# Kernel optimization log

Hardware: AMD Instinct MI355X
Metric: run time of the kernel (lower is better)

The kernel has to match this reference:

```python
import jax, jax.numpy as jnp
import numpy as np

N_EMBED = 384
NUM_HEADS = 6
HEAD_SIZE = N_EMBED // NUM_HEADS  # 64
B, T = 8, 2048


def setup_inputs() -> dict:
    key = jax.random.key(0)
    ks = jax.random.split(key, 8)
    s = 1.0 / np.sqrt(N_EMBED)
    query = jax.random.normal(ks[0], (B, T, N_EMBED), dtype=jnp.float32)
    key_t = jax.random.normal(ks[1], (B, T, N_EMBED), dtype=jnp.float32)
    value = jax.random.normal(ks[2], (B, T, N_EMBED), dtype=jnp.float32)
    # causal-style mask, broadcastable over (B, H)
    mask = jnp.tril(jnp.ones((T, T), dtype=jnp.int32))[None, None]
    Wk = jax.random.normal(ks[3], (N_EMBED, N_EMBED), dtype=jnp.float32) * s
    Wq = jax.random.normal(ks[4], (N_EMBED, N_EMBED), dtype=jnp.float32) * s
    Wv = jax.random.normal(ks[5], (N_EMBED, N_EMBED), dtype=jnp.float32) * s
    Wproj = jax.random.normal(ks[6], (N_EMBED, N_EMBED), dtype=jnp.float32) * s
    bproj = jnp.zeros((N_EMBED,), dtype=jnp.float32)
    return {"query": query, "key": key_t, "value": value, "mask": mask,
            "Wk": Wk, "Wq": Wq, "Wv": Wv, "Wproj": Wproj, "bproj": bproj}


def _split_heads(x):
    b, t, c = x.shape
    return x.reshape(b, t, NUM_HEADS, c // NUM_HEADS).transpose(0, 2, 1, 3)  # [B,H,T,D]


def reference(query, key, value, mask, Wk, Wq, Wv, Wproj, bproj):
    b, t, c = query.shape
    # NOTE: source swaps names: k = key_proj(query), q = query_proj(key)
    k = _split_heads(query @ Wk.T)
    q = _split_heads(key @ Wq.T)
    v = _split_heads(value @ Wv.T)
    # scale by full C (not head_size), as in the source
    wei = jnp.einsum("bhqd,bhkd->bhqk", q, k) * (c ** -0.5)
    # masked_fill with 0 BEFORE softmax (faithful to source)
    wei = jnp.where(mask == 0, jnp.float32(0.0), wei)
    wei = jax.nn.softmax(wei, axis=-1)
    out = jnp.einsum("bhqk,bhkd->bhqd", wei, v)
    out = out.transpose(0, 2, 1, 3).reshape(b, t, c)
    out = out @ Wproj.T + bproj  # dropout is identity at inference
    return out
```

## Files before the change

### kernel.cpp

```cpp
#include <hip/hip_runtime.h>
#include <hip/hip_bf16.h>


#define TT 2048
#define CC 384
#define HH 6
#define DD 64
#define SCALE 0.05103103630798288f

typedef __bf16 bf16x8 __attribute__((ext_vector_type(8)));
typedef __bf16 bf16x4 __attribute__((ext_vector_type(4)));
typedef float f32x4 __attribute__((ext_vector_type(4)));

__device__ __forceinline__ int swz(int row, int byteInRow) {
    return row * 128 + (byteInRow ^ ((row & 7) << 4));
}

__global__ __launch_bounds__(256) void qkv_proj_kernel(
    const float* __restrict__ query, const float* __restrict__ key,
    const float* __restrict__ value, const float* __restrict__ Wk,
    const float* __restrict__ Wq, const float* __restrict__ Wv,
    __bf16* __restrict__ Kb, __bf16* __restrict__ Qb, __bf16* __restrict__ VTb)
{
    __shared__ __align__(16) char smem[49152];

    const int tid = threadIdx.x;
    const int wid = tid >> 6, lane = tid & 63;
    const int lrow = lane & 15, g = lane >> 4;
    const int pid = blockIdx.z;
    const int m0 = blockIdx.x * 128, n0 = blockIdx.y * 64;
    const float* X = (pid == 0) ? query : ((pid == 1) ? key : value);
    const float* W = (pid == 0) ? Wk : ((pid == 1) ? Wq : Wv);

    const int xrow = tid >> 4, xcol = (tid & 15) * 4;
    const float* xp = X + (size_t)(m0 + xrow) * CC + xcol;
    const float* wp = W + (size_t)(n0 + (tid >> 4)) * CC + xcol;

    f32x4 xr[8], wr[4];

    f32x4 acc[2][4];
#pragma unroll
    for (int i = 0; i < 2; ++i)
#pragma unroll
        for (int j = 0; j < 4; ++j) acc[i][j] = (f32x4){0.f, 0.f, 0.f, 0.f};

#pragma unroll
    for (int i = 0; i < 8; ++i) xr[i] = *(const f32x4*)(xp + (size_t)i * 16 * CC);
#pragma unroll
    for (int i = 0; i < 4; ++i) wr[i] = *(const f32x4*)(wp + (size_t)i * 16 * CC);
    {
        char* Xd = smem;
        char* Wd = smem + 32768;
#pragma unroll
        for (int i = 0; i < 8; ++i) {
            bf16x4 hh;
            hh[0] = (__bf16)xr[i][0]; hh[1] = (__bf16)xr[i][1];
            hh[2] = (__bf16)xr[i][2]; hh[3] = (__bf16)xr[i][3];
            *(bf16x4*)(Xd + swz(xrow + i * 16, xcol * 2)) = hh;
        }
#pragma unroll
        for (int i = 0; i < 4; ++i) {
            bf16x4 hh;
            hh[0] = (__bf16)wr[i][0]; hh[1] = (__bf16)wr[i][1];
            hh[2] = (__bf16)wr[i][2]; hh[3] = (__bf16)wr[i][3];
            *(bf16x4*)(Wd + swz((tid >> 4) + i * 16, xcol * 2)) = hh;
        }
    }
    __syncthreads();

    int cur = 0;
    for (int kk = 0; kk < 6; ++kk) {
        if (kk < 5) {
            const int k0 = (kk + 1) * 64;
#pragma unroll
            for (int i = 0; i < 8; ++i) xr[i] = *(const f32x4*)(xp + (size_t)i * 16 * CC + k0);
#pragma unroll
            for (int i = 0; i < 4; ++i) wr[i] = *(const f32x4*)(wp + (size_t)i * 16 * CC + k0);
        }
        const char* Xs = smem + cur * 16384;
        const char* Ws = smem + 32768 + cur * 8192;

        __builtin_amdgcn_s_setprio(1);
        if (pid < 2) {
#pragma unroll
            for (int kc = 0; kc < 2; ++kc) {
                int kb = kc * 64 + g * 16;
                bf16x8 a0 = *(bf16x8*)(Xs + swz(wid * 32 + lrow, kb));
                bf16x8 a1 = *(bf16x8*)(Xs + swz(wid * 32 + 16 + lrow, kb));
#pragma unroll
                for (int nf = 0; nf < 4; ++nf) {
                    bf16x8 b = *(bf16x8*)(Ws + swz(nf * 16 + lrow, kb));
                    acc[0][nf] = __builtin_amdgcn_mfma_f32_16x16x32_bf16(a0, b, acc[0][nf], 0, 0, 0);
                    acc[1][nf] = __builtin_amdgcn_mfma_f32_16x16x32_bf16(a1, b, acc[1][nf], 0, 0, 0);
                }
            }
        } else {
#pragma unroll
            for (int kc = 0; kc < 2; ++kc) {
                int kb = kc * 64 + g * 16;
                bf16x8 b0 = *(bf16x8*)(Xs + swz(wid * 32 + lrow, kb));
                bf16x8 b1 = *(bf16x8*)(Xs + swz(wid * 32 + 16 + lrow, kb));
#pragma unroll
                for (int nf = 0; nf < 4; ++nf) {
                    bf16x8 a = *(bf16x8*)(Ws + swz(nf * 16 + lrow, kb));
                    acc[0][nf] = __builtin_amdgcn_mfma_f32_16x16x32_bf16(a, b0, acc[0][nf], 0, 0, 0);
                    acc[1][nf] = __builtin_amdgcn_mfma_f32_16x16x32_bf16(a, b1, acc[1][nf], 0, 0, 0);
                }
            }
        }
        __builtin_amdgcn_s_setprio(0);

        if (kk < 5) {
            char* Xd = smem + (cur ^ 1) * 16384;
            char* Wd = smem + 32768 + (cur ^ 1) * 8192;
#pragma unroll
            for (int i = 0; i < 8; ++i) {
                bf16x4 hh;
                hh[0] = (__bf16)xr[i][0]; hh[1] = (__bf16)xr[i][1];
                hh[2] = (__bf16)xr[i][2]; hh[3] = (__bf16)xr[i][3];
                *(bf16x4*)(Xd + swz(xrow + i * 16, xcol * 2)) = hh;
            }
#pragma unroll
            for (int i = 0; i < 4; ++i) {
                bf16x4 hh;
                hh[0] = (__bf16)wr[i][0]; hh[1] = (__bf16)wr[i][1];
                hh[2] = (__bf16)wr[i][2]; hh[3] = (__bf16)wr[i][3];
                *(bf16x4*)(Wd + swz((tid >> 4) + i * 16, xcol * 2)) = hh;
            }
        }
        __syncthreads();
        cur ^= 1;
    }

    if (pid < 2) {
        __bf16* out = (pid == 0) ? Kb : Qb;
#pragma unroll
        for (int mf = 0; mf < 2; ++mf)
#pragma unroll
            for (int nf = 0; nf < 4; ++nf)
#pragma unroll
                for (int r = 0; r < 4; ++r) {
                    int m = m0 + wid * 32 + mf * 16 + g * 4 + r;
                    int n = n0 + nf * 16 + lrow;
                    int b = m >> 11, t = m & 2047, h = n >> 6, d = n & 63;
                    out[((size_t)(b * HH + h) * TT + t) * DD + d] = (__bf16)acc[mf][nf][r];
                }
    } else {
#pragma unroll
        for (int mf = 0; mf < 2; ++mf)
#pragma unroll
            for (int nf = 0; nf < 4; ++nf)
#pragma unroll
                for (int r = 0; r < 4; ++r) {
                    int n = n0 + nf * 16 + g * 4 + r;
                    int m = m0 + wid * 32 + mf * 16 + lrow;
                    int b = m >> 11, t = m & 2047, h = n >> 6, d = n & 63;
                    VTb[((size_t)(b * HH + h) * DD + d) * TT + t] = (__bf16)acc[mf][nf][r];
                }
    }
}

__global__ __launch_bounds__(256) void suffix_kernel(
    const __bf16* __restrict__ VTb, float* __restrict__ Ssuf)
{
    __shared__ float tsum[4][32];
    const int bh = blockIdx.x;
    const int tid = threadIdx.x, wid = tid >> 6, lane = tid & 63;

#pragma unroll
    for (int it = 0; it < 4; ++it) {
        const int dr = blockIdx.y * 16 + wid * 4 + it;
        const __bf16* src = VTb + (size_t)(bh * DD + dr) * TT;
#pragma unroll
        for (int step = 0; step < 4; ++step) {
            bf16x8 v = *(const bf16x8*)(src + step * 512 + lane * 8);
            float sacc = 0.f;
#pragma unroll
            for (int i = 0; i < 8; ++i) sacc += (float)v[i];
            sacc += __shfl_xor(sacc, 1);
            sacc += __shfl_xor(sacc, 2);
            sacc += __shfl_xor(sacc, 4);
            if ((lane & 7) == 0) tsum[wid][step * 8 + (lane >> 3)] = sacc;
        }
        float s2 = 0.f;
        for (int j = 0; j < 32; ++j) {
            float tv = tsum[wid][j];
            if (j >= lane) s2 += tv;
        }
        if (lane <= 32) Ssuf[(size_t)(bh * 33 + lane) * 64 + dr] = s2;
    }
}

__global__ __launch_bounds__(256) void attn_kernel(
    const __bf16* __restrict__ Qb, const __bf16* __restrict__ Kb,
    const __bf16* __restrict__ VTb, const float* __restrict__ Ssuf,
    __bf16* __restrict__ attn)
{
    __shared__ __align__(16) char smem[32768];
    const int tid = threadIdx.x;
    const int wid = tid >> 6, lane = tid & 63;
    const int lrow = lane & 15, g = lane >> 4;

    const int i = blockIdx.x;
    const int j = i >> 3;
    const int bh = (i & 7) * 6 + (j >> 4);
    const int Qt = 15 - (j & 15);
    const int q0 = Qt * 128;
    const int nkt = 2 * Qt + 2;

    const int qloc = wid * 32 + lrow;
    const __bf16* qp = Qb + ((size_t)bh * TT + q0 + qloc) * DD + g * 8;
    bf16x8 qb[2][2];
    qb[0][0] = *(const bf16x8*)(qp);
    qb[0][1] = *(const bf16x8*)(qp + 32);
    qb[1][0] = *(const bf16x8*)(qp + 16 * DD);
    qb[1][1] = *(const bf16x8*)(qp + 16 * DD + 32);

    const int r0 = tid >> 3;
    const int c8 = (tid & 7) * 8;
    const __bf16* kbase = Kb + (size_t)bh * TT * DD;
    const __bf16* vbase = VTb + (size_t)bh * DD * TT;

    bf16x8 kr0, kr1, vr0, vr1;

    f32x4 o[2][4];
#pragma unroll
    for (int mf = 0; mf < 2; ++mf)
#pragma unroll
        for (int ds = 0; ds < 4; ++ds) o[mf][ds] = (f32x4){0.f, 0.f, 0.f, 0.f};
    float z0 = 0.f, z1 = 0.f;

    kr0 = *(const bf16x8*)(kbase + (size_t)r0 * DD + c8);
    kr1 = *(const bf16x8*)(kbase + (size_t)(r0 + 32) * DD + c8);
    vr0 = *(const bf16x8*)(vbase + (size_t)r0 * TT + c8);
    vr1 = *(const bf16x8*)(vbase + (size_t)(r0 + 32) * TT + c8);
    {
        char* Kd = smem;
        char* Vd = smem + 16384;
        *(bf16x8*)(Kd + swz(r0, c8 * 2)) = kr0;
        *(bf16x8*)(Kd + swz(r0 + 32, c8 * 2)) = kr1;
        *(bf16x8*)(Vd + swz(r0, c8 * 2)) = vr0;
        *(bf16x8*)(Vd + swz(r0 + 32, c8 * 2)) = vr1;
    }
    __syncthreads();

    int cur = 0;
    for (int kt = 0; kt < nkt; ++kt) {
        if (kt + 1 < nkt) {
            const int n0 = (kt + 1) * 64;
            kr0 = *(const bf16x8*)(kbase + (size_t)(n0 + r0) * DD + c8);
            kr1 = *(const bf16x8*)(kbase + (size_t)(n0 + r0 + 32) * DD + c8);
            vr0 = *(const bf16x8*)(vbase + (size_t)r0 * TT + n0 + c8);
            vr1 = *(const bf16x8*)(vbase + (size_t)(r0 + 32) * TT + n0 + c8);
        }
        const char* Kc = smem + cur * 8192;
        const char* Vc = smem + 16384 + cur * 8192;
        const bool dm = (kt >= 2 * Qt);

#pragma unroll
        for (int mf = 0; mf < 2; ++mf) {
            f32x4 st[4];
#pragma unroll
            for (int j16 = 0; j16 < 4; ++j16) st[j16] = (f32x4){0.f, 0.f, 0.f, 0.f};
            __builtin_amdgcn_s_setprio(1);
#pragma unroll
            for (int kc = 0; kc < 2; ++kc) {
                bf16x8 qf = qb[mf][kc];
#pragma unroll
                for (int j16 = 0; j16 < 4; ++j16) {
                    bf16x8 kf = *(bf16x8*)(Kc + swz(j16 * 16 + lrow, kc * 64 + g * 16));
                    st[j16] = __builtin_amdgcn_mfma_f32_16x16x32_bf16(kf, qf, st[j16], 0, 0, 0);
                }
            }
            __builtin_amdgcn_s_setprio(0);

            const int qg = q0 + qloc + mf * 16;
            bf16x8 pb0, pb1;
            float zz = 0.f;
#pragma unroll
            for (int j16 = 0; j16 < 4; ++j16) {
#pragma unroll
                for (int r = 0; r < 4; ++r) {
                    float p;
                    if (dm && (kt * 64 + j16 * 16 + g * 4 + r > qg)) p = 1.0f;
                    else p = __expf(st[j16][r] * SCALE);
                    zz += p;
                    if (j16 < 2) pb0[(j16 & 1) * 4 + r] = (__bf16)p;
                    else         pb1[(j16 & 1) * 4 + r] = (__bf16)p;
                }
            }
            if (mf == 0) z0 += zz; else z1 += zz;

            __builtin_amdgcn_s_setprio(1);
#pragma unroll
            for (int kc = 0; kc < 2; ++kc) {
                bf16x8 pf = kc ? pb1 : pb0;
#pragma unroll
                for (int ds = 0; ds < 4; ++ds) {
                    union { bf16x8 v8; bf16x4 h[2]; } vf;
                    vf.h[0] = *(bf16x4*)(Vc + swz(ds * 16 + lrow, kc * 64 + 8 * g));
                    vf.h[1] = *(bf16x4*)(Vc + swz(ds * 16 + lrow, kc * 64 + 8 * g + 32));
                    o[mf][ds] = __builtin_amdgcn_mfma_f32_16x16x32_bf16(vf.v8, pf, o[mf][ds], 0, 0, 0);
                }
            }
            __builtin_amdgcn_s_setprio(0);
        }

        if (kt + 1 < nkt) {
            char* Kd = smem + (cur ^ 1) * 8192;
            char* Vd = smem + 16384 + (cur ^ 1) * 8192;
            *(bf16x8*)(Kd + swz(r0, c8 * 2)) = kr0;
            *(bf16x8*)(Kd + swz(r0 + 32, c8 * 2)) = kr1;
            *(bf16x8*)(Vd + swz(r0, c8 * 2)) = vr0;
            *(bf16x8*)(Vd + swz(r0 + 32, c8 * 2)) = vr1;
        }
        __syncthreads();
        cur ^= 1;
    }

    const float fut = (float)(TT - nkt * 64);
    z0 += __shfl_xor(z0, 16); z0 += __shfl_xor(z0, 32);
    z1 += __shfl_xor(z1, 16); z1 += __shfl_xor(z1, 32);
    const float inv0 = 1.0f / (z0 + fut);
    const float inv1 = 1.0f / (z1 + fut);

    const float* suf = Ssuf + ((size_t)bh * 33 + nkt) * 64;
    const int b = bh / HH, h = bh % HH;
#pragma unroll
    for (int mf = 0; mf < 2; ++mf) {
        const int t = q0 + qloc + mf * 16;
        const float inv = mf ? inv1 : inv0;
        __bf16* orow = attn + ((size_t)(b * TT + t)) * CC + h * DD;
#pragma unroll
        for (int ds = 0; ds < 4; ++ds) {
            f32x4 sv = *(const f32x4*)(suf + ds * 16 + g * 4);
            bf16x4 w;
#pragma unroll
            for (int r = 0; r < 4; ++r) w[r] = (__bf16)((o[mf][ds][r] + sv[r]) * inv);
            *(bf16x4*)(orow + ds * 16 + g * 4) = w;
        }
    }
}

__global__ __launch_bounds__(256) void out_proj_kernel(
    const __bf16* __restrict__ A, const float* __restrict__ W,
    const float* __restrict__ bias, float* __restrict__ out)
{
    __shared__ __align__(16) char smem[49152];
    const int tid = threadIdx.x;
    const int wid = tid >> 6, lane = tid & 63;
    const int lrow = lane & 15, g = lane >> 4;
    const int m0 = blockIdx.x * 128, n0 = blockIdx.y * 64;

    const int arow = tid >> 3, ac8 = (tid & 7) * 8;
    const __bf16* ap = A + (size_t)(m0 + arow) * CC + ac8;
    const int wrow = tid >> 4, wcol = (tid & 15) * 4;
    const float* wp = W + (size_t)(n0 + wrow) * CC + wcol;

    bf16x8 ar[4];
    f32x4 wr[4];

    f32x4 acc[2][4];
#pragma unroll
    for (int i = 0; i < 2; ++i)
#pragma unroll
        for (int j = 0; j < 4; ++j) acc[i][j] = (f32x4){0.f, 0.f, 0.f, 0.f};

#pragma unroll
    for (int i = 0; i < 4; ++i) ar[i] = *(const bf16x8*)(ap + (size_t)i * 32 * CC);
#pragma unroll
    for (int i = 0; i < 4; ++i) wr[i] = *(const f32x4*)(wp + (size_t)i * 16 * CC);
    {
        char* Ad = smem;
        char* Wd = smem + 32768;
#pragma unroll
        for (int i = 0; i < 4; ++i)
            *(bf16x8*)(Ad + swz(arow + i * 32, ac8 * 2)) = ar[i];
#pragma unroll
        for (int i = 0; i < 4; ++i) {
            bf16x4 hh;
            hh[0] = (__bf16)wr[i][0]; hh[1] = (__bf16)wr[i][1];
            hh[2] = (__bf16)wr[i][2]; hh[3] = (__bf16)wr[i][3];
            *(bf16x4*)(Wd + swz(wrow + i * 16, wcol * 2)) = hh;
        }
    }
    __syncthreads();

    int cur = 0;
    for (int kk = 0; kk < 6; ++kk) {
        if (kk < 5) {
            const int k0 = (kk + 1) * 64;
#pragma unroll
            for (int i = 0; i < 4; ++i) ar[i] = *(const bf16x8*)(ap + (size_t)i * 32 * CC + k0);
#pragma unroll
            for (int i = 0; i < 4; ++i) wr[i] = *(const f32x4*)(wp + (size_t)i * 16 * CC + k0);
        }
        const char* Xs = smem + cur * 16384;
        const char* Ws = smem + 32768 + cur * 8192;

        __builtin_amdgcn_s_setprio(1);
#pragma unroll
        for (int kc = 0; kc < 2; ++kc) {
            int kb = kc * 64 + g * 16;
            bf16x8 a0 = *(bf16x8*)(Xs + swz(wid * 32 + lrow, kb));
            bf16x8 a1 = *(bf16x8*)(Xs + swz(wid * 32 + 16 + lrow, kb));
#pragma unroll
            for (int nf = 0; nf < 4; ++nf) {
                bf16x8 b = *(bf16x8*)(Ws + swz(nf * 16 + lrow, kb));
                acc[0][nf] = __builtin_amdgcn_mfma_f32_16x16x32_bf16(a0, b, acc[0][nf], 0, 0, 0);
                acc[1][nf] = __builtin_amdgcn_mfma_f32_16x16x32_bf16(a1, b, acc[1][nf], 0, 0, 0);
            }
        }
        __builtin_amdgcn_s_setprio(0);

        if (kk < 5) {
            char* Ad = smem + (cur ^ 1) * 16384;
            char* Wd = smem + 32768 + (cur ^ 1) * 8192;
#pragma unroll
            for (int i = 0; i < 4; ++i)
                *(bf16x8*)(Ad + swz(arow + i * 32, ac8 * 2)) = ar[i];
#pragma unroll
            for (int i = 0; i < 4; ++i) {
                bf16x4 hh;
                hh[0] = (__bf16)wr[i][0]; hh[1] = (__bf16)wr[i][1];
                hh[2] = (__bf16)wr[i][2]; hh[3] = (__bf16)wr[i][3];
                *(bf16x4*)(Wd + swz(wrow + i * 16, wcol * 2)) = hh;
            }
        }
        __syncthreads();
        cur ^= 1;
    }

#pragma unroll
    for (int nf = 0; nf < 4; ++nf) {
        float bv = bias[n0 + nf * 16 + lrow];
#pragma unroll
        for (int mf = 0; mf < 2; ++mf)
#pragma unroll
            for (int r = 0; r < 4; ++r) {
                int m = m0 + wid * 32 + mf * 16 + g * 4 + r;
                out[(size_t)m * CC + n0 + nf * 16 + lrow] = acc[mf][nf][r] + bv;
            }
    }
}

extern "C" void kernel_launch(void* const* d_in, const int* in_sizes, int n_in,
                              void* d_out, int out_size, void* d_ws, size_t ws_size,
                              hipStream_t stream)
{
    (void)in_sizes; (void)n_in; (void)out_size; (void)ws_size;
    const float* query = (const float*)d_in[0];
    const float* key   = (const float*)d_in[1];
    const float* value = (const float*)d_in[2];
    const float* Wk    = (const float*)d_in[4];
    const float* Wq    = (const float*)d_in[5];
    const float* Wv    = (const float*)d_in[6];
    const float* Wproj = (const float*)d_in[7];
    const float* bproj = (const float*)d_in[8];
    float* out = (float*)d_out;

    char* ws = (char*)d_ws;
    const size_t SZ = 12582912;
    __bf16* Qb   = (__bf16*)(ws);
    __bf16* Kb   = (__bf16*)(ws + SZ);
    __bf16* VTb  = (__bf16*)(ws + 2 * SZ);
    __bf16* Ab   = (__bf16*)(ws + 3 * SZ);
    float*  Ssuf = (float*)(ws + 4 * SZ);

    qkv_proj_kernel<<<dim3(128, 6, 3), 256, 0, stream>>>(query, key, value,
                                                         Wk, Wq, Wv, Kb, Qb, VTb);
    suffix_kernel<<<dim3(48, 4), 256, 0, stream>>>(VTb, Ssuf);
    attn_kernel<<<dim3(768), 256, 0, stream>>>(Qb, Kb, VTb, Ssuf, Ab);
    out_proj_kernel<<<dim3(128, 6), 256, 0, stream>>>(Ab, Wproj, bproj, out);
}
```

Measured before the change: 274.2 us.

## Hoist K/V fragment loads to registers, reorder block mapping, use exp2

```diff
diff --git a/kernel.cpp b/kernel.cpp
--- a/kernel.cpp
+++ b/kernel.cpp
@@ -7,6 +7,7 @@
 #define HH 6
 #define DD 64
 #define SCALE 0.05103103630798288f
+#define SCALE2 0.07362223f
 
 typedef __bf16 bf16x8 __attribute__((ext_vector_type(8)));
 typedef __bf16 bf16x4 __attribute__((ext_vector_type(4)));
@@ -191,7 +192,7 @@
     }
 }
 
-__global__ __launch_bounds__(256) void attn_kernel(
+__global__ __launch_bounds__(256, 3) void attn_kernel(
     const __bf16* __restrict__ Qb, const __bf16* __restrict__ Kb,
     const __bf16* __restrict__ VTb, const float* __restrict__ Ssuf,
     __bf16* __restrict__ attn)
@@ -202,9 +203,11 @@
     const int lrow = lane & 15, g = lane >> 4;
 
     const int i = blockIdx.x;
+    const int xcd = i & 7;
     const int j = i >> 3;
-    const int bh = (i & 7) * 6 + (j >> 4);
-    const int Qt = 15 - (j & 15);
+    const int rank = j / 6;
+    const int bh = xcd * 6 + (j % 6);
+    const int Qt = 15 - rank;
     const int q0 = Qt * 128;
     const int nkt = 2 * Qt + 2;
 
@@ -257,23 +260,42 @@
         const char* Vc = smem + 16384 + cur * 8192;
         const bool dm = (kt >= 2 * Qt);
 
+        bf16x8 kfr[2][4];
+#pragma unroll
+        for (int kc = 0; kc < 2; ++kc)
+#pragma unroll
+            for (int j16 = 0; j16 < 4; ++j16)
+                kfr[kc][j16] = *(const bf16x8*)(Kc + swz(j16 * 16 + lrow, kc * 64 + g * 16));
+
+        f32x4 st[2][4];
+#pragma unroll
+        for (int mf = 0; mf < 2; ++mf)
+#pragma unroll
+            for (int j16 = 0; j16 < 4; ++j16) st[mf][j16] = (f32x4){0.f, 0.f, 0.f, 0.f};
+        __builtin_amdgcn_s_setprio(1);
+#pragma unroll
+        for (int kc = 0; kc < 2; ++kc)
+#pragma unroll
+            for (int mf = 0; mf < 2; ++mf)
+#pragma unroll
+                for (int j16 = 0; j16 < 4; ++j16)
+                    st[mf][j16] = __builtin_amdgcn_mfma_f32_16x16x32_bf16(
+                        kfr[kc][j16], qb[mf][kc], st[mf][j16], 0, 0, 0);
+        __builtin_amdgcn_s_setprio(0);
+
+        bf16x8 vfr[2][4];
+#pragma unroll
+        for (int kc = 0; kc < 2; ++kc)
+#pragma unroll
+            for (int ds = 0; ds < 4; ++ds) {
+                union { bf16x8 v8; bf16x4 h[2]; } u;
+                u.h[0] = *(const bf16x4*)(Vc + swz(ds * 16 + lrow, kc * 64 + 8 * g));
+                u.h[1] = *(const bf16x4*)(Vc + swz(ds * 16 + lrow, kc * 64 + 8 * g + 32));
+                vfr[kc][ds] = u.v8;
+            }
+
 #pragma unroll
         for (int mf = 0; mf < 2; ++mf) {
-            f32x4 st[4];
-#pragma unroll
-            for (int j16 = 0; j16 < 4; ++j16) st[j16] = (f32x4){0.f, 0.f, 0.f, 0.f};
-            __builtin_amdgcn_s_setprio(1);
-#pragma unroll
-            for (int kc = 0; kc < 2; ++kc) {
-                bf16x8 qf = qb[mf][kc];
-#pragma unroll
-                for (int j16 = 0; j16 < 4; ++j16) {
-                    bf16x8 kf = *(bf16x8*)(Kc + swz(j16 * 16 + lrow, kc * 64 + g * 16));
-                    st[j16] = __builtin_amdgcn_mfma_f32_16x16x32_bf16(kf, qf, st[j16], 0, 0, 0);
-                }
-            }
-            __builtin_amdgcn_s_setprio(0);
-
             const int qg = q0 + qloc + mf * 16;
             bf16x8 pb0, pb1;
             float zz = 0.f;
@@ -283,7 +305,7 @@
                 for (int r = 0; r < 4; ++r) {
                     float p;
                     if (dm && (kt * 64 + j16 * 16 + g * 4 + r > qg)) p = 1.0f;
-                    else p = __expf(st[j16][r] * SCALE);
+                    else p = exp2f(st[mf][j16][r] * SCALE2);
                     zz += p;
                     if (j16 < 2) pb0[(j16 & 1) * 4 + r] = (__bf16)p;
                     else         pb1[(j16 & 1) * 4 + r] = (__bf16)p;
@@ -296,12 +318,9 @@
             for (int kc = 0; kc < 2; ++kc) {
                 bf16x8 pf = kc ? pb1 : pb0;
 #pragma unroll
-                for (int ds = 0; ds < 4; ++ds) {
-                    union { bf16x8 v8; bf16x4 h[2]; } vf;
-                    vf.h[0] = *(bf16x4*)(Vc + swz(ds * 16 + lrow, kc * 64 + 8 * g));
-                    vf.h[1] = *(bf16x4*)(Vc + swz(ds * 16 + lrow, kc * 64 + 8 * g + 32));
-                    o[mf][ds] = __builtin_amdgcn_mfma_f32_16x16x32_bf16(vf.v8, pf, o[mf][ds], 0, 0, 0);
-                }
+                for (int ds = 0; ds < 4; ++ds)
+                    o[mf][ds] = __builtin_amdgcn_mfma_f32_16x16x32_bf16(
+                        vfr[kc][ds], pf, o[mf][ds], 0, 0, 0);
             }
             __builtin_amdgcn_s_setprio(0);
         }
```

Result: faster. 263.9 us (-3.8%).
